# Performance work log

Hardware: AMD Instinct MI355X
Metric: run time of the kernel (lower is better)

The kernel has to match this reference:

```python
import jax, jax.numpy as jnp
import numpy as np
import math

DIM_IN = 2048
QDIM = 2048
RATIO = 2
LATENT = DIM_IN // RATIO  # 1024
N_ROIS = 4096
N_BANK = 8192
LN_EPS = 1e-5


def setup_inputs() -> dict:
    key = jax.random.key(0)
    ks = jax.random.split(key, 20)
    s = 0.02
    inp = {
        "feat": jax.random.normal(ks[0], (N_ROIS, QDIM), jnp.float32),
        "key_bank": jax.random.normal(ks[1], (N_BANK, DIM_IN), jnp.float32),
        # branch 1 (projectc*) weights, torch Linear convention [out, in]
        "Wc1": jax.random.normal(ks[2], (LATENT, QDIM), jnp.float32) * s,
        "bc1": jax.random.normal(ks[3], (LATENT,), jnp.float32) * s,
        "Wc2": jax.random.normal(ks[4], (LATENT, DIM_IN), jnp.float32) * s,
        "bc2": jax.random.normal(ks[5], (LATENT,), jnp.float32) * s,
        "Wc3": jax.random.normal(ks[6], (LATENT, DIM_IN), jnp.float32) * s,
        "bc3": jax.random.normal(ks[7], (LATENT,), jnp.float32) * s,
        # branch 2 (projectd*)
        "Wd1": jax.random.normal(ks[8], (LATENT, QDIM), jnp.float32) * s,
        "bd1": jax.random.normal(ks[9], (LATENT,), jnp.float32) * s,
        "Wd2": jax.random.normal(ks[10], (LATENT, DIM_IN), jnp.float32) * s,
        "bd2": jax.random.normal(ks[11], (LATENT,), jnp.float32) * s,
        "Wd3": jax.random.normal(ks[12], (LATENT, DIM_IN), jnp.float32) * s,
        "bd3": jax.random.normal(ks[13], (LATENT,), jnp.float32) * s,
        # cffn: LayerNorm(latent) -> PReLU -> Linear(latent, dim_in) (dropout = identity in eval)
        "ln_w": jnp.ones((LATENT,), jnp.float32),
        "ln_b": jnp.zeros((LATENT,), jnp.float32),
        "prelu_a": jnp.full((1,), 0.25, jnp.float32),
        "Wffn": jax.random.normal(ks[14], (DIM_IN, LATENT), jnp.float32) * s,
        "bffn": jax.random.normal(ks[15], (DIM_IN,), jnp.float32) * s,
    }
    return inp


def _attn_branch(q, k, v):
    # q: [N, L], k/v: [M, L] -> [N, L]
    scores = jnp.einsum("nl,ml->nm", q, k) / math.sqrt(LATENT)
    p = jax.nn.softmax(scores, axis=-1)
    return jnp.einsum("nm,ml->nl", p, v)


def reference(feat, key_bank, Wc1, bc1, Wc2, bc2, Wc3, bc3,
              Wd1, bd1, Wd2, bd2, Wd3, bd3,
              ln_w, ln_b, prelu_a, Wffn, bffn):
    # projections (torch Linear: x @ W.T + b)
    q1 = feat @ Wc1.T + bc1
    k1 = key_bank @ Wc2.T + bc2
    v1 = key_bank @ Wc3.T + bc3
    q2 = feat @ Wd1.T + bd1
    k2 = key_bank @ Wd2.T + bd2
    v2 = key_bank @ Wd3.T + bd3

    f1 = _attn_branch(q1, k1, v1)
    f2 = _attn_branch(q2, k2, v2)
    cpair = f1 * f2  # elementwise gating of the two attention branches

    # cffn: LayerNorm -> PReLU -> Linear (dropout is identity at inference)
    mu = jnp.mean(cpair, axis=-1, keepdims=True)
    var = jnp.mean(jnp.square(cpair - mu), axis=-1, keepdims=True)
    x = (cpair - mu) * jax.lax.rsqrt(var + LN_EPS) * ln_w + ln_b
    x = jnp.where(x >= 0, x, prelu_a * x)  # PReLU, single shared slope
    out = x @ Wffn.T + bffn  # [N, dim_in]
    return out
```

## Files before the change

kernel.cpp:

```cpp
#include <hip/hip_runtime.h>
#include <cstdint>

typedef _Float16 f16;
typedef __attribute__((ext_vector_type(8))) _Float16 f16x8;
typedef __attribute__((ext_vector_type(4))) _Float16 f16x4;
typedef __attribute__((ext_vector_type(4))) float f32x4;

#define NROIS 4096
#define NBANK 8192
#define DIMIN 2048
#define LAT   1024

__device__ __forceinline__ void gload16(const f16* g, f16* l) {
  __builtin_amdgcn_global_load_lds(
      (const __attribute__((address_space(1))) void*)g,
      (__attribute__((address_space(3))) void*)l, 16, 0, 0);
}

__device__ __forceinline__ f32x4 mfma16(f16x8 a, f16x8 b, f32x4 c) {
  return __builtin_amdgcn_mfma_f32_16x16x32_f16(a, b, c, 0, 0, 0);
}

#define A_BSTR ((size_t)2048 * 8192)
#define B_BSTR ((size_t)1024 * 8192)
#define C_BSTR ((size_t)4194304)

template<int MODE>
__global__ __launch_bounds__(512, 1)
void gemm2(const f16* __restrict__ A, const f16* __restrict__ B,
           void* __restrict__ Cp, int K, int lda, int ldb, int ldc,
           const float* __restrict__ bias, float* __restrict__ den,
           float scale)
{
  extern __shared__ __align__(16) f16 lds[];
  f16* As = lds;
  f16* Bs = lds + 4 * 8192;

  const int tid  = threadIdx.x;
  const int w    = tid >> 6;
  const int lane = tid & 63;

  int br = 0, sp = blockIdx.z;
  if (MODE == 4) { br = blockIdx.z >> 2; sp = blockIdx.z & 3; }
  const f16* Abase_g = A;
  const f16* Bbase_g = B;
  if (MODE == 4) { Abase_g += (size_t)br * A_BSTR; Bbase_g += (size_t)br * B_BSTR; }

  const int gx = gridDim.x;
  const int nwg = gx * gridDim.y;
  int id = blockIdx.y * gx + blockIdx.x;
  id = (id & 7) * (nwg >> 3) + (id >> 3);
  const int bx = id % gx, by = id / gx;

  const int r0   = by * 256;
  const int c0   = bx * 256;
  const int koff = sp * K;

  const int rr = tid >> 2;
  const int ci = (tid & 3) ^ ((tid >> 3) & 3);
  const f16* gA = Abase_g + (size_t)(r0 + rr) * lda + koff + ci * 8;
  const f16* gB = Bbase_g + (size_t)(c0 + rr) * ldb + koff + ci * 8;
  const size_t lda128 = (size_t)128 * lda;
  const size_t ldb128 = (size_t)128 * ldb;
  f16* dA = As + tid * 8;
  f16* dB = Bs + tid * 8;

  const int swz  = ((lane >> 4) ^ ((lane >> 1) & 3)) * 8;
  const int aoff = ((w >> 2) * 128 + (lane & 15)) * 32 + swz;
  const int boff = ((w & 3) * 64 + (lane & 15)) * 32 + swz;

  f32x4 acc[8][4];
#pragma unroll
  for (int m = 0; m < 8; ++m)
#pragma unroll
    for (int n = 0; n < 4; ++n)
      acc[m][n] = (f32x4)0.0f;

  const int nt = K >> 5;

  gload16(gA,               dA);
  gload16(gA + lda128,      dA + 4096);
  gload16(gB,               dB);
  gload16(gB + ldb128,      dB + 4096);
  gload16(gA + 32,          dA + 8192);
  gload16(gA + 32 + lda128, dA + 8192 + 4096);
  gload16(gB + 32,          dB + 8192);
  gload16(gB + 32 + ldb128, dB + 8192 + 4096);
  asm volatile("s_waitcnt vmcnt(4)" ::: "memory");
  __builtin_amdgcn_s_barrier();
  __builtin_amdgcn_sched_barrier(0);

  for (int t = 0; t < nt; ++t) {
    const int s = (t & 3) * 8192;
    const f16* Ab = As + s + aoff;
    const f16* Bb = Bs + s + boff;
    const bool pf = (t + 2) < nt;
    if (pf) {
      const int ps = ((t + 2) & 3) * 8192;
      const f16* gAt = gA + (size_t)(t + 2) * 32;
      const f16* gBt = gB + (size_t)(t + 2) * 32;
      gload16(gAt,          dA + ps);
      gload16(gAt + lda128, dA + ps + 4096);
      gload16(gBt,          dB + ps);
      gload16(gBt + ldb128, dB + ps + 4096);
    }
    f16x8 af[8], bf[4];
#pragma unroll
    for (int n = 0; n < 4; ++n) bf[n] = *(const f16x8*)(Bb + n * 512);
#pragma unroll
    for (int m = 0; m < 8; ++m) af[m] = *(const f16x8*)(Ab + m * 512);
    __builtin_amdgcn_s_setprio(1);
#pragma unroll
    for (int m = 0; m < 8; ++m)
#pragma unroll
      for (int n = 0; n < 4; ++n)
        acc[m][n] = mfma16(af[m], bf[n], acc[m][n]);
    __builtin_amdgcn_s_setprio(0);
    __builtin_amdgcn_sched_barrier(0);
    if (pf) asm volatile("s_waitcnt vmcnt(4)" ::: "memory");
    else    asm volatile("s_waitcnt vmcnt(0)" ::: "memory");
    __builtin_amdgcn_s_barrier();
    __builtin_amdgcn_sched_barrier(0);
  }

  const int cr = (lane >> 4) * 4;
  const int cc = lane & 15;
  const int wrow = (w >> 2) * 128;
  const int wcol = (w & 3) * 64;

  if (MODE == 0) {
    f16* C = (f16*)Cp;
    float bv[4];
#pragma unroll
    for (int n = 0; n < 4; ++n) bv[n] = bias[c0 + wcol + n * 16 + cc];
#pragma unroll
    for (int m = 0; m < 8; ++m)
#pragma unroll
      for (int j = 0; j < 4; ++j) {
        const int r = r0 + wrow + m * 16 + cr + j;
#pragma unroll
        for (int n = 0; n < 4; ++n) {
          const int c = c0 + wcol + n * 16 + cc;
          C[(size_t)r * ldc + c] = (f16)(acc[m][n][j] + bv[n]);
        }
      }
  } else if (MODE == 1) {
    f16* C = (f16*)Cp;
#pragma unroll
    for (int m = 0; m < 8; ++m)
#pragma unroll
      for (int j = 0; j < 4; ++j) {
        const int r = r0 + wrow + m * 16 + cr + j;
        float rs = 0.0f;
#pragma unroll
        for (int n = 0; n < 4; ++n) {
          const int c = c0 + wcol + n * 16 + cc;
          float e = __expf(acc[m][n][j] * scale);
          rs += e;
          C[(size_t)r * ldc + c] = (f16)e;
        }
        rs += __shfl_xor(rs, 1);
        rs += __shfl_xor(rs, 2);
        rs += __shfl_xor(rs, 4);
        rs += __shfl_xor(rs, 8);
        if (cc == 0) unsafeAtomicAdd(&den[r], rs);
      }
  } else {
    float* C = (float*)Cp;
    if (MODE == 4) C += (size_t)br * C_BSTR;
#pragma unroll
    for (int m = 0; m < 8; ++m)
#pragma unroll
      for (int j = 0; j < 4; ++j) {
        const int r = r0 + wrow + m * 16 + cr + j;
#pragma unroll
        for (int n = 0; n < 4; ++n) {
          const int c = c0 + wcol + n * 16 + cc;
          unsafeAtomicAdd(&C[(size_t)r * ldc + c], acc[m][n][j]);
        }
      }
  }
}

template<int MODE>
__global__ __launch_bounds__(256)
void gemm_bt(const f16* __restrict__ A, const f16* __restrict__ B,
             void* __restrict__ Cp, int K, int lda, int ldb, int ldc,
             const float* __restrict__ bias, float* __restrict__ den,
             float scale)
{
  __shared__ __align__(16) f16 As[128 * 32];
  __shared__ __align__(16) f16 Bs[128 * 32];
  const int t    = threadIdx.x;
  const int w    = t >> 6;
  const int lane = t & 63;
  const int r0   = blockIdx.y * 128;
  const int c0   = blockIdx.x * 128;
  const int koff = blockIdx.z * K;

  const int lr = lane >> 2;
  const int lc = ((lane & 3) ^ ((lane >> 3) & 3)) * 8;

  f32x4 acc[4][4];
#pragma unroll
  for (int m = 0; m < 4; ++m)
#pragma unroll
    for (int n = 0; n < 4; ++n)
      acc[m][n] = (f32x4)0.0f;

  const int wr = (w >> 1) * 64;
  const int wc = (w & 1) * 64;
  const int fr = lane & 15;
  const int fs = ((lane >> 4) ^ ((lane >> 1) & 3)) * 8;

  for (int k0 = 0; k0 < K; k0 += 32) {
#pragma unroll
    for (int i = 0; i < 2; ++i) {
      const int ch = i * 4 + w;
      gload16(A + (size_t)(r0 + ch * 16 + lr) * lda + (koff + k0 + lc),
              &As[ch * 512 + lane * 8]);
      gload16(B + (size_t)(c0 + ch * 16 + lr) * ldb + (koff + k0 + lc),
              &Bs[ch * 512 + lane * 8]);
    }
    __syncthreads();

    f16x8 af[4], bfv[4];
#pragma unroll
    for (int m = 0; m < 4; ++m)
      af[m] = *(const f16x8*)&As[(wr + m * 16 + fr) * 32 + fs];
#pragma unroll
    for (int n = 0; n < 4; ++n)
      bfv[n] = *(const f16x8*)&Bs[(wc + n * 16 + fr) * 32 + fs];
#pragma unroll
    for (int m = 0; m < 4; ++m)
#pragma unroll
      for (int n = 0; n < 4; ++n)
        acc[m][n] = mfma16(af[m], bfv[n], acc[m][n]);
    __syncthreads();
  }

  const int cr = (lane >> 4) * 4;
  const int cc = lane & 15;

  if (MODE == 0) {
    f16* C = (f16*)Cp;
#pragma unroll
    for (int m = 0; m < 4; ++m)
#pragma unroll
      for (int j = 0; j < 4; ++j) {
        const int r = r0 + wr + m * 16 + cr + j;
#pragma unroll
        for (int n = 0; n < 4; ++n) {
          const int c = c0 + wc + n * 16 + cc;
          C[(size_t)r * ldc + c] = (f16)(acc[m][n][j] + bias[c]);
        }
      }
  } else {
    float* C = (float*)Cp;
#pragma unroll
    for (int m = 0; m < 4; ++m)
#pragma unroll
      for (int j = 0; j < 4; ++j) {
        const int r = r0 + wr + m * 16 + cr + j;
#pragma unroll
        for (int n = 0; n < 4; ++n) {
          const int c = c0 + wc + n * 16 + cc;
          C[(size_t)r * ldc + c] = acc[m][n][j] + bias[c];
        }
      }
  }
}

__global__ __launch_bounds__(256)
void cvt_f16(const float* __restrict__ in, f16* __restrict__ out, int n4) {
  int i = blockIdx.x * 256 + threadIdx.x;
  const int stride = gridDim.x * 256;
  for (; i < n4; i += stride) {
    float4 v = ((const float4*)in)[i];
    f16x4 o = { (f16)v.x, (f16)v.y, (f16)v.z, (f16)v.w };
    ((f16x4*)out)[i] = o;
  }
}

__global__ __launch_bounds__(256)
void init_misc(const float* __restrict__ bc1, const float* __restrict__ bd1,
               const float* __restrict__ bc2, const float* __restrict__ bc3,
               const float* __restrict__ bd2, const float* __restrict__ bd3,
               float* __restrict__ biasq, float* __restrict__ biaskv,
               float* __restrict__ den)
{
  const int i = blockIdx.x * 256 + threadIdx.x;
  if (i < 1024) {
    biasq[i]         = bc1[i];
    biasq[1024 + i]  = bd1[i];
    biaskv[i]        = bc2[i];
    biaskv[1024 + i] = bc3[i];
    biaskv[2048 + i] = bd2[i];
    biaskv[3072 + i] = bd3[i];
  }
  den[i] = 0.0f;
}

__global__ __launch_bounds__(256)
void zero_f32(float4* __restrict__ p, int n4) {
  int i = blockIdx.x * 256 + threadIdx.x;
  const int stride = gridDim.x * 256;
  float4 z; z.x = 0.f; z.y = 0.f; z.z = 0.f; z.w = 0.f;
  for (; i < n4; i += stride) p[i] = z;
}

__global__ __launch_bounds__(256)
void fill_f32(float* __restrict__ p, float v, int n) {
  int i = blockIdx.x * 256 + threadIdx.x;
  const int stride = gridDim.x * 256;
  for (; i < n; i += stride) p[i] = v;
}

__global__ __launch_bounds__(256)
void transpose_v(const f16* __restrict__ kv, f16* __restrict__ vT, int col_ofs) {
  __shared__ f16 tile[64][66];
  const int r0 = blockIdx.x * 64;
  const int c0 = blockIdx.y * 64;
  const int tx = threadIdx.x;
  const int ty = threadIdx.y;
  for (int i = ty; i < 64; i += 4)
    tile[i][tx] = kv[(size_t)(r0 + i) * 4096 + col_ofs + c0 + tx];
  __syncthreads();
  for (int i = ty; i < 64; i += 4)
    vT[(size_t)(c0 + i) * NBANK + r0 + tx] = tile[tx][i];
}

__global__ __launch_bounds__(256)
void gate_ln(const float* __restrict__ f1, const float* __restrict__ f2,
             const float* __restrict__ den,
             const float* __restrict__ lnw, const float* __restrict__ lnb,
             const float* __restrict__ pa, f16* __restrict__ x)
{
  const int row = blockIdx.x;
  const int t   = threadIdx.x;
  const int lane = t & 63, w = t >> 6;
  const float inv1 = 1.0f / den[row];
  const float inv2 = 1.0f / den[NROIS + row];
  const float4 a = ((const float4*)(f1 + (size_t)row * LAT))[t];
  const float4 b = ((const float4*)(f2 + (size_t)row * LAT))[t];
  float c[4] = { a.x * b.x * inv1 * inv2, a.y * b.y * inv1 * inv2,
                 a.z * b.z * inv1 * inv2, a.w * b.w * inv1 * inv2 };
  float s = c[0] + c[1] + c[2] + c[3];
  float q = c[0]*c[0] + c[1]*c[1] + c[2]*c[2] + c[3]*c[3];
#pragma unroll
  for (int m = 1; m < 64; m <<= 1) {
    s += __shfl_xor(s, m);
    q += __shfl_xor(q, m);
  }
  __shared__ float red[8];
  if (lane == 0) { red[w] = s; red[4 + w] = q; }
  __syncthreads();
  s = red[0] + red[1] + red[2] + red[3];
  q = red[4] + red[5] + red[6] + red[7];
  const float mu  = s * (1.0f / LAT);
  const float var = q * (1.0f / LAT) - mu * mu;
  const float rs  = rsqrtf(var + 1e-5f);
  const float slope = pa[0];
  f16x4 o;
#pragma unroll
  for (int j = 0; j < 4; ++j) {
    float xv = (c[j] - mu) * rs * lnw[t * 4 + j] + lnb[t * 4 + j];
    xv = (xv >= 0.0f) ? xv : slope * xv;
    o[j] = (f16)xv;
  }
  ((f16x4*)(x + (size_t)row * LAT))[t] = o;
}

extern "C" void kernel_launch(void* const* d_in, const int* in_sizes, int n_in,
                              void* d_out, int out_size, void* d_ws, size_t ws_size,
                              hipStream_t stream) {
  const float* feat = (const float*)d_in[0];
  const float* bank = (const float*)d_in[1];
  const float* Wc1  = (const float*)d_in[2];
  const float* bc1  = (const float*)d_in[3];
  const float* Wc2  = (const float*)d_in[4];
  const float* bc2  = (const float*)d_in[5];
  const float* Wc3  = (const float*)d_in[6];
  const float* bc3  = (const float*)d_in[7];
  const float* Wd1  = (const float*)d_in[8];
  const float* bd1  = (const float*)d_in[9];
  const float* Wd2  = (const float*)d_in[10];
  const float* bd2  = (const float*)d_in[11];
  const float* Wd3  = (const float*)d_in[12];
  const float* bd3  = (const float*)d_in[13];
  const float* lnw  = (const float*)d_in[14];
  const float* lnb  = (const float*)d_in[15];
  const float* pa   = (const float*)d_in[16];
  const float* Wffn = (const float*)d_in[17];
  const float* bffn = (const float*)d_in[18];

  const size_t MBy = 1ull << 20;

  if (ws_size < 133 * MBy) {
    fill_f32<<<dim3(2048), dim3(256), 0, stream>>>((float*)d_out, 12345.0f, out_size);
    return;
  }
  const bool big = ws_size >= 181 * MBy;

  const int DYN_LDS = 4 * 2 * 8192 * 2;
  (void)hipFuncSetAttribute(reinterpret_cast<const void*>(&gemm2<0>),
                            hipFuncAttributeMaxDynamicSharedMemorySize, DYN_LDS);
  (void)hipFuncSetAttribute(reinterpret_cast<const void*>(&gemm2<1>),
                            hipFuncAttributeMaxDynamicSharedMemorySize, DYN_LDS);
  (void)hipFuncSetAttribute(reinterpret_cast<const void*>(&gemm2<2>),
                            hipFuncAttributeMaxDynamicSharedMemorySize, DYN_LDS);
  (void)hipFuncSetAttribute(reinterpret_cast<const void*>(&gemm2<4>),
                            hipFuncAttributeMaxDynamicSharedMemorySize, DYN_LDS);

  char* ws = (char*)d_ws;
  f16* kvb = (f16*)(ws);
  f16* q12 = (f16*)(ws + 64 * MBy);
  f16* Wfb = (f16*)(ws + 80 * MBy);
  f16* WQ  = (f16*)(ws + 84 * MBy);
  f16* xbuf = (f16*)(ws + 84 * MBy);
  f16*   WKV = (f16*)d_out;
  f16*   FB  = (f16*)((char*)d_out + 16 * MBy);
  float* f1  = (float*)d_out;
  float* f2  = (float*)((char*)d_out + 16 * MBy);

  f16 *vT0, *vT1 = nullptr, *E0, *E1 = nullptr, *BB;
  float *biasq, *biaskv, *den;
  if (big) {
    vT0 = (f16*)(ws + 84 * MBy);
    vT1 = (f16*)(ws + 100 * MBy);
    E0  = (f16*)(ws + 116 * MBy);
    E1  = (f16*)(ws + 148 * MBy);
    BB  = (f16*)(ws + 116 * MBy);
    biasq  = (float*)(ws + 180 * MBy);
    biaskv = (float*)(ws + 180 * MBy + 8192);
    den    = (float*)(ws + 180 * MBy + 24576);
  } else {
    vT0 = (f16*)(ws + 84 * MBy);
    E0  = (f16*)(ws + 100 * MBy);
    BB  = (f16*)(ws + 92 * MBy);
    biasq  = (float*)(ws + 132 * MBy);
    biaskv = (float*)(ws + 132 * MBy + 8192);
    den    = (float*)(ws + 132 * MBy + 24576);
  }

  init_misc<<<dim3(32), dim3(256), 0, stream>>>(bc1, bd1, bc2, bc3, bd2, bd3,
                                                biasq, biaskv, den);

  auto cvt = [&](const float* in, f16* out, size_t n) {
    int n4 = (int)(n / 4);
    int blocks = (n4 + 255) / 256;
    if (blocks > 2048) blocks = 2048;
    cvt_f16<<<dim3(blocks), dim3(256), 0, stream>>>(in, out, n4);
  };
  cvt(Wc1, WQ,                          (size_t)1024 * 2048);
  cvt(Wd1, WQ + (size_t)1024 * 2048,    (size_t)1024 * 2048);
  cvt(feat, FB, (size_t)NROIS * DIMIN);
  cvt(Wc2, WKV,                         (size_t)1024 * 2048);
  cvt(Wc3, WKV + (size_t)1024 * 2048,   (size_t)1024 * 2048);
  cvt(Wd2, WKV + (size_t)2048 * 2048,   (size_t)1024 * 2048);
  cvt(Wd3, WKV + (size_t)3072 * 2048,   (size_t)1024 * 2048);
  cvt(bank, BB, (size_t)NBANK * DIMIN);
  cvt(Wffn, Wfb, (size_t)2048 * 1024);

  gemm_bt<0><<<dim3(16, 32, 1), 256, 0, stream>>>(
      FB, WQ, q12, 2048, 2048, 2048, 2048, biasq, nullptr, 0.0f);
  gemm2<0><<<dim3(16, 32, 1), 512, DYN_LDS, stream>>>(
      BB, WKV, kvb, 2048, 2048, 2048, 4096, biaskv, nullptr, 0.0f);

  zero_f32<<<dim3(2048), dim3(256), 0, stream>>>((float4*)d_out, (32 * (int)MBy) / 16);

  const float scl = 0.03125f;
  if (big) {
    transpose_v<<<dim3(128, 16, 1), dim3(64, 4), 0, stream>>>(kvb, vT0, 1024);
    transpose_v<<<dim3(128, 16, 1), dim3(64, 4), 0, stream>>>(kvb, vT1, 3072);
    for (int chunk = 0; chunk < 2; ++chunk) {
      const size_t qo = (size_t)chunk * 2048 * 2048;
      gemm2<1><<<dim3(32, 8, 1), 512, DYN_LDS, stream>>>(
          q12 + qo, kvb, E0, 1024, 2048, 4096, 8192,
          nullptr, den + chunk * 2048, scl);
      gemm2<1><<<dim3(32, 8, 1), 512, DYN_LDS, stream>>>(
          q12 + qo + 1024, kvb + 2048, E1, 1024, 2048, 4096, 8192,
          nullptr, den + NROIS + chunk * 2048, scl);
      gemm2<4><<<dim3(4, 8, 8), 512, DYN_LDS, stream>>>(
          E0, vT0, f1 + (size_t)chunk * 2048 * 1024, 2048, 8192, 8192, 1024,
          nullptr, nullptr, 0.0f);
    }
  } else {
    for (int b = 0; b < 2; ++b) {
      transpose_v<<<dim3(128, 16, 1), dim3(64, 4), 0, stream>>>(
          kvb, vT0, 1024 + b * 2048);
      float* fb = b ? f2 : f1;
      for (int chunk = 0; chunk < 2; ++chunk) {
        gemm2<1><<<dim3(32, 8, 1), 512, DYN_LDS, stream>>>(
            q12 + (size_t)chunk * 2048 * 2048 + b * 1024, kvb + b * 2048,
            E0, 1024, 2048, 4096, 8192,
            nullptr, den + b * NROIS + chunk * 2048, scl);
        gemm2<2><<<dim3(4, 8, 4), 512, DYN_LDS, stream>>>(
            E0, vT0, fb + (size_t)chunk * 2048 * 1024, 2048, 8192, 8192, 1024,
            nullptr, nullptr, 0.0f);
      }
    }
  }

  gate_ln<<<dim3(NROIS), dim3(256), 0, stream>>>(f1, f2, den, lnw, lnb, pa, xbuf);

  gemm_bt<3><<<dim3(16, 32, 1), 256, 0, stream>>>(
      xbuf, Wfb, (float*)d_out, 1024, 1024, 1024, 2048, bffn, nullptr, 0.0f);
}
```

Measured before the change: 932.1 us.

## Split GEMM main loop into two halves, batch conversions, add large-workspace tier

The gemm2 main loop now loads and computes the A fragments in two halves. A barrier sits between the halves, and the global-to-LDS prefetch is split across them so memory traffic interleaves with MFMA work and fewer fragment registers are live at once. The nine fp32-to-fp16 conversion launches are merged into one multi-segment kernel to cut launch overhead. A new workspace tier, used when the workspace is large enough, runs the attention score and PV GEMMs over all 4096 rows in single launches instead of two chunks. The extra barrier per k-step and the per-element segment search in the conversion kernel add some overhead in exchange.

```diff
diff --git a/kernel.cpp b/kernel.cpp
--- a/kernel.cpp
+++ b/kernel.cpp
@@ -20,17 +20,15 @@
 __device__ __forceinline__ f32x4 mfma16(f16x8 a, f16x8 b, f32x4 c) {
   return __builtin_amdgcn_mfma_f32_16x16x32_f16(a, b, c, 0, 0, 0);
 }
-
-#define A_BSTR ((size_t)2048 * 8192)
-#define B_BSTR ((size_t)1024 * 8192)
-#define C_BSTR ((size_t)4194304)
 
 template<int MODE>
 __global__ __launch_bounds__(512, 1)
 void gemm2(const f16* __restrict__ A, const f16* __restrict__ B,
            void* __restrict__ Cp, int K, int lda, int ldb, int ldc,
            const float* __restrict__ bias, float* __restrict__ den,
-           float scale)
+           float scale, int zlog,
+           unsigned long long aBstr, unsigned long long bBstr,
+           unsigned long long cBstr)
 {
   extern __shared__ __align__(16) f16 lds[];
   f16* As = lds;
@@ -41,10 +39,10 @@
   const int lane = tid & 63;
 
   int br = 0, sp = blockIdx.z;
-  if (MODE == 4) { br = blockIdx.z >> 2; sp = blockIdx.z & 3; }
+  if (MODE == 4) { br = blockIdx.z >> zlog; sp = blockIdx.z & ((1 << zlog) - 1); }
   const f16* Abase_g = A;
   const f16* Bbase_g = B;
-  if (MODE == 4) { Abase_g += (size_t)br * A_BSTR; Bbase_g += (size_t)br * B_BSTR; }
+  if (MODE == 4) { Abase_g += (size_t)br * aBstr; Bbase_g += (size_t)br * bBstr; }
 
   const int gx = gridDim.x;
   const int nwg = gx * gridDim.y;
@@ -95,26 +93,42 @@
     const f16* Ab = As + s + aoff;
     const f16* Bb = Bs + s + boff;
     const bool pf = (t + 2) < nt;
+    const int ps = ((t + 2) & 3) * 8192;
+    const f16* gAt = gA + (size_t)(t + 2) * 32;
+    const f16* gBt = gB + (size_t)(t + 2) * 32;
+
+    f16x8 af[4], bf[4];
+#pragma unroll
+    for (int n = 0; n < 4; ++n) bf[n] = *(const f16x8*)(Bb + n * 512);
+#pragma unroll
+    for (int m = 0; m < 4; ++m) af[m] = *(const f16x8*)(Ab + m * 512);
     if (pf) {
-      const int ps = ((t + 2) & 3) * 8192;
-      const f16* gAt = gA + (size_t)(t + 2) * 32;
-      const f16* gBt = gB + (size_t)(t + 2) * 32;
       gload16(gAt,          dA + ps);
       gload16(gAt + lda128, dA + ps + 4096);
+    }
+    __builtin_amdgcn_s_setprio(1);
+#pragma unroll
+    for (int m = 0; m < 4; ++m)
+#pragma unroll
+      for (int n = 0; n < 4; ++n)
+        acc[m][n] = mfma16(af[m], bf[n], acc[m][n]);
+    __builtin_amdgcn_s_setprio(0);
+    __builtin_amdgcn_sched_barrier(0);
+    __builtin_amdgcn_s_barrier();
+    __builtin_amdgcn_sched_barrier(0);
+
+#pragma unroll
+    for (int m = 0; m < 4; ++m) af[m] = *(const f16x8*)(Ab + (m + 4) * 512);
+    if (pf) {
       gload16(gBt,          dB + ps);
       gload16(gBt + ldb128, dB + ps + 4096);
     }
-    f16x8 af[8], bf[4];
-#pragma unroll
-    for (int n = 0; n < 4; ++n) bf[n] = *(const f16x8*)(Bb + n * 512);
-#pragma unroll
-    for (int m = 0; m < 8; ++m) af[m] = *(const f16x8*)(Ab + m * 512);
     __builtin_amdgcn_s_setprio(1);
 #pragma unroll
-    for (int m = 0; m < 8; ++m)
+    for (int m = 0; m < 4; ++m)
 #pragma unroll
       for (int n = 0; n < 4; ++n)
-        acc[m][n] = mfma16(af[m], bf[n], acc[m][n]);
+        acc[m + 4][n] = mfma16(af[m], bf[n], acc[m + 4][n]);
     __builtin_amdgcn_s_setprio(0);
     __builtin_amdgcn_sched_barrier(0);
     if (pf) asm volatile("s_waitcnt vmcnt(4)" ::: "memory");
@@ -167,7 +181,7 @@
       }
   } else {
     float* C = (float*)Cp;
-    if (MODE == 4) C += (size_t)br * C_BSTR;
+    if (MODE == 4) C += (size_t)br * cBstr;
 #pragma unroll
     for (int m = 0; m < 8; ++m)
 #pragma unroll
@@ -186,8 +200,7 @@
 __global__ __launch_bounds__(256)
 void gemm_bt(const f16* __restrict__ A, const f16* __restrict__ B,
              void* __restrict__ Cp, int K, int lda, int ldb, int ldc,
-             const float* __restrict__ bias, float* __restrict__ den,
-             float scale)
+             const float* __restrict__ bias)
 {
   __shared__ __align__(16) f16 As[128 * 32];
   __shared__ __align__(16) f16 Bs[128 * 32];
@@ -196,7 +209,6 @@
   const int lane = t & 63;
   const int r0   = blockIdx.y * 128;
   const int c0   = blockIdx.x * 128;
-  const int koff = blockIdx.z * K;
 
   const int lr = lane >> 2;
   const int lc = ((lane & 3) ^ ((lane >> 3) & 3)) * 8;
@@ -217,9 +229,9 @@
 #pragma unroll
     for (int i = 0; i < 2; ++i) {
       const int ch = i * 4 + w;
-      gload16(A + (size_t)(r0 + ch * 16 + lr) * lda + (koff + k0 + lc),
+      gload16(A + (size_t)(r0 + ch * 16 + lr) * lda + (k0 + lc),
               &As[ch * 512 + lane * 8]);
-      gload16(B + (size_t)(c0 + ch * 16 + lr) * ldb + (koff + k0 + lc),
+      gload16(B + (size_t)(c0 + ch * 16 + lr) * ldb + (k0 + lc),
               &Bs[ch * 512 + lane * 8]);
     }
     __syncthreads();
@@ -271,14 +283,19 @@
   }
 }
 
-__global__ __launch_bounds__(256)
-void cvt_f16(const float* __restrict__ in, f16* __restrict__ out, int n4) {
+struct CvtSeg { const float* src; f16* dst; int n4; };
+struct CvtArgs { CvtSeg s[9]; int tot4; };
+
+__global__ __launch_bounds__(256)
+void cvt_multi(CvtArgs a) {
   int i = blockIdx.x * 256 + threadIdx.x;
   const int stride = gridDim.x * 256;
-  for (; i < n4; i += stride) {
-    float4 v = ((const float4*)in)[i];
+  for (; i < a.tot4; i += stride) {
+    int j = i, k = 0;
+    while (j >= a.s[k].n4) { j -= a.s[k].n4; ++k; }
+    float4 v = ((const float4*)a.s[k].src)[j];
     f16x4 o = { (f16)v.x, (f16)v.y, (f16)v.z, (f16)v.w };
-    ((f16x4*)out)[i] = o;
+    ((f16x4*)a.s[k].dst)[j] = o;
   }
 }
 
@@ -400,7 +417,7 @@
     fill_f32<<<dim3(2048), dim3(256), 0, stream>>>((float*)d_out, 12345.0f, out_size);
     return;
   }
-  const bool big = ws_size >= 181 * MBy;
+  const int tier = (ws_size >= 245 * MBy) ? 2 : (ws_size >= 181 * MBy) ? 1 : 0;
 
   const int DYN_LDS = 4 * 2 * 8192 * 2;
   (void)hipFuncSetAttribute(reinterpret_cast<const void*>(&gemm2<0>),
@@ -413,10 +430,10 @@
                             hipFuncAttributeMaxDynamicSharedMemorySize, DYN_LDS);
 
   char* ws = (char*)d_ws;
-  f16* kvb = (f16*)(ws);
-  f16* q12 = (f16*)(ws + 64 * MBy);
-  f16* Wfb = (f16*)(ws + 80 * MBy);
-  f16* WQ  = (f16*)(ws + 84 * MBy);
+  f16* kvb  = (f16*)(ws);
+  f16* q12  = (f16*)(ws + 64 * MBy);
+  f16* Wfb  = (f16*)(ws + 80 * MBy);
+  f16* WQ   = (f16*)(ws + 84 * MBy);
   f16* xbuf = (f16*)(ws + 84 * MBy);
   f16*   WKV = (f16*)d_out;
   f16*   FB  = (f16*)((char*)d_out + 16 * MBy);
@@ -425,65 +442,84 @@
 
   f16 *vT0, *vT1 = nullptr, *E0, *E1 = nullptr, *BB;
   float *biasq, *biaskv, *den;
-  if (big) {
+  size_t tail;
+  if (tier == 2) {
+    vT0 = (f16*)(ws + 84 * MBy);
+    vT1 = (f16*)(ws + 100 * MBy);
+    E0  = (f16*)(ws + 116 * MBy);
+    E1  = (f16*)(ws + 180 * MBy);
+    BB  = (f16*)(ws + 116 * MBy);
+    tail = 244 * MBy;
+  } else if (tier == 1) {
     vT0 = (f16*)(ws + 84 * MBy);
     vT1 = (f16*)(ws + 100 * MBy);
     E0  = (f16*)(ws + 116 * MBy);
     E1  = (f16*)(ws + 148 * MBy);
     BB  = (f16*)(ws + 116 * MBy);
-    biasq  = (float*)(ws + 180 * MBy);
-    biaskv = (float*)(ws + 180 * MBy + 8192);
-    den    = (float*)(ws + 180 * MBy + 24576);
+    tail = 180 * MBy;
   } else {
     vT0 = (f16*)(ws + 84 * MBy);
     E0  = (f16*)(ws + 100 * MBy);
     BB  = (f16*)(ws + 92 * MBy);
-    biasq  = (float*)(ws + 132 * MBy);
-    biaskv = (float*)(ws + 132 * MBy + 8192);
-    den    = (float*)(ws + 132 * MBy + 24576);
-  }
+    tail = 132 * MBy;
+  }
+  biasq  = (float*)(ws + tail);
+  biaskv = (float*)(ws + tail + 8192);
+  den    = (float*)(ws + tail + 24576);
 
   init_misc<<<dim3(32), dim3(256), 0, stream>>>(bc1, bd1, bc2, bc3, bd2, bd3,
                                                 biasq, biaskv, den);
 
-  auto cvt = [&](const float* in, f16* out, size_t n) {
-    int n4 = (int)(n / 4);
-    int blocks = (n4 + 255) / 256;
-    if (blocks > 2048) blocks = 2048;
-    cvt_f16<<<dim3(blocks), dim3(256), 0, stream>>>(in, out, n4);
-  };
-  cvt(Wc1, WQ,                          (size_t)1024 * 2048);
-  cvt(Wd1, WQ + (size_t)1024 * 2048,    (size_t)1024 * 2048);
-  cvt(feat, FB, (size_t)NROIS * DIMIN);
-  cvt(Wc2, WKV,                         (size_t)1024 * 2048);
-  cvt(Wc3, WKV + (size_t)1024 * 2048,   (size_t)1024 * 2048);
-  cvt(Wd2, WKV + (size_t)2048 * 2048,   (size_t)1024 * 2048);
-  cvt(Wd3, WKV + (size_t)3072 * 2048,   (size_t)1024 * 2048);
-  cvt(bank, BB, (size_t)NBANK * DIMIN);
-  cvt(Wffn, Wfb, (size_t)2048 * 1024);
+  {
+    CvtArgs a;
+    const int W4 = (1024 * 2048) / 4;
+    a.s[0] = { Wc1,  WQ,                         W4 };
+    a.s[1] = { Wd1,  WQ + (size_t)1024 * 2048,   W4 };
+    a.s[2] = { feat, FB,                         (NROIS * DIMIN) / 4 };
+    a.s[3] = { Wc2,  WKV,                        W4 };
+    a.s[4] = { Wc3,  WKV + (size_t)1024 * 2048,  W4 };
+    a.s[5] = { Wd2,  WKV + (size_t)2048 * 2048,  W4 };
+    a.s[6] = { Wd3,  WKV + (size_t)3072 * 2048,  W4 };
+    a.s[7] = { bank, BB,                         (NBANK * DIMIN) / 4 };
+    a.s[8] = { Wffn, Wfb,                        W4 };
+    a.tot4 = 7 * W4 + (NROIS * DIMIN) / 4 + (NBANK * DIMIN) / 4;
+    cvt_multi<<<dim3(2048), dim3(256), 0, stream>>>(a);
+  }
 
   gemm_bt<0><<<dim3(16, 32, 1), 256, 0, stream>>>(
-      FB, WQ, q12, 2048, 2048, 2048, 2048, biasq, nullptr, 0.0f);
+      FB, WQ, q12, 2048, 2048, 2048, 2048, biasq);
   gemm2<0><<<dim3(16, 32, 1), 512, DYN_LDS, stream>>>(
-      BB, WKV, kvb, 2048, 2048, 2048, 4096, biaskv, nullptr, 0.0f);
+      BB, WKV, kvb, 2048, 2048, 2048, 4096, biaskv, nullptr, 0.0f, 0, 0, 0, 0);
 
   zero_f32<<<dim3(2048), dim3(256), 0, stream>>>((float4*)d_out, (32 * (int)MBy) / 16);
 
   const float scl = 0.03125f;
-  if (big) {
+  if (tier == 2) {
+    transpose_v<<<dim3(128, 16, 1), dim3(64, 4), 0, stream>>>(kvb, vT0, 1024);
+    transpose_v<<<dim3(128, 16, 1), dim3(64, 4), 0, stream>>>(kvb, vT1, 3072);
+    gemm2<1><<<dim3(32, 16, 1), 512, DYN_LDS, stream>>>(
+        q12, kvb, E0, 1024, 2048, 4096, 8192, nullptr, den, scl, 0, 0, 0, 0);
+    gemm2<1><<<dim3(32, 16, 1), 512, DYN_LDS, stream>>>(
+        q12 + 1024, kvb + 2048, E1, 1024, 2048, 4096, 8192,
+        nullptr, den + NROIS, scl, 0, 0, 0, 0);
+    gemm2<4><<<dim3(4, 16, 4), 512, DYN_LDS, stream>>>(
+        E0, vT0, f1, 4096, 8192, 8192, 1024, nullptr, nullptr, 0.0f,
+        1, (size_t)4096 * 8192, (size_t)1024 * 8192, (size_t)4096 * 1024);
+  } else if (tier == 1) {
     transpose_v<<<dim3(128, 16, 1), dim3(64, 4), 0, stream>>>(kvb, vT0, 1024);
     transpose_v<<<dim3(128, 16, 1), dim3(64, 4), 0, stream>>>(kvb, vT1, 3072);
     for (int chunk = 0; chunk < 2; ++chunk) {
       const size_t qo = (size_t)chunk * 2048 * 2048;
       gemm2<1><<<dim3(32, 8, 1), 512, DYN_LDS, stream>>>(
           q12 + qo, kvb, E0, 1024, 2048, 4096, 8192,
-          nullptr, den + chunk * 2048, scl);
+          nullptr, den + chunk * 2048, scl, 0, 0, 0, 0);
       gemm2<1><<<dim3(32, 8, 1), 512, DYN_LDS, stream>>>(
           q12 + qo + 1024, kvb + 2048, E1, 1024, 2048, 4096, 8192,
-          nullptr, den + NROIS + chunk * 2048, scl);
+          nullptr, den + NROIS + chunk * 2048, scl, 0, 0, 0, 0);
       gemm2<4><<<dim3(4, 8, 8), 512, DYN_LDS, stream>>>(
           E0, vT0, f1 + (size_t)chunk * 2048 * 1024, 2048, 8192, 8192, 1024,
-          nullptr, nullptr, 0.0f);
+          nullptr, nullptr, 0.0f,
+          2, (size_t)2048 * 8192, (size_t)1024 * 8192, (size_t)4096 * 1024);
     }
   } else {
     for (int b = 0; b < 2; ++b) {
@@ -494,10 +530,10 @@
         gemm2<1><<<dim3(32, 8, 1), 512, DYN_LDS, stream>>>(
             q12 + (size_t)chunk * 2048 * 2048 + b * 1024, kvb + b * 2048,
             E0, 1024, 2048, 4096, 8192,
-            nullptr, den + b * NROIS + chunk * 2048, scl);
+            nullptr, den + b * NROIS + chunk * 2048, scl, 0, 0, 0, 0);
         gemm2<2><<<dim3(4, 8, 4), 512, DYN_LDS, stream>>>(
             E0, vT0, fb + (size_t)chunk * 2048 * 1024, 2048, 8192, 8192, 1024,
-            nullptr, nullptr, 0.0f);
+            nullptr, nullptr, 0.0f, 0, 0, 0, 0);
       }
     }
   }
@@ -505,5 +541,5 @@
   gate_ln<<<dim3(NROIS), dim3(256), 0, stream>>>(f1, f2, den, lnw, lnb, pa, xbuf);
 
   gemm_bt<3><<<dim3(16, 32, 1), 256, 0, stream>>>(
-      xbuf, Wfb, (float*)d_out, 1024, 1024, 1024, 2048, bffn, nullptr, 0.0f);
-}
+      xbuf, Wfb, (float*)d_out, 1024, 1024, 1024, 2048, bffn);
+}
```

Result: faster. 882.7 us (-5.3%).
